# Optimization experiments

Measured on AMD Instinct MI355X. Metric: run time of the kernel, lower is better.

Reference implementation:

```python
import jax, jax.numpy as jnp
import numpy as np

N_DRUG, N_PROT = 20000, 8000
D_DRUG, D_PROT = 300, 1280
HIDDEN, OUT = 512, 5
N_EDGE, N_LBL = 500000, 200000


def setup_inputs() -> dict:
    key = jax.random.key(0)
    ks = jax.random.split(key, 12)
    inp = {
        "x_drug": jax.random.normal(ks[0], (N_DRUG, D_DRUG), dtype=jnp.float32),
        "x_prot": jax.random.normal(ks[1], (N_PROT, D_PROT), dtype=jnp.float32),
        "edge_src": jax.random.randint(ks[2], (N_EDGE,), 0, N_DRUG, dtype=jnp.int32),
        "edge_dst": jax.random.randint(ks[3], (N_EDGE,), 0, N_PROT, dtype=jnp.int32),
        "lbl_src": jax.random.randint(ks[4], (N_LBL,), 0, N_DRUG, dtype=jnp.int32),
        "lbl_dst": jax.random.randint(ks[5], (N_LBL,), 0, N_PROT, dtype=jnp.int32),
        # SAGEConv params: lin_l (on aggregated src msgs, with bias), lin_r (on dst, no bias)
        "W_l": jax.random.normal(ks[6], (HIDDEN, D_DRUG), dtype=jnp.float32) / np.sqrt(D_DRUG),
        "b_l": jnp.zeros((HIDDEN,), dtype=jnp.float32),
        "W_r": jax.random.normal(ks[7], (HIDDEN, D_PROT), dtype=jnp.float32) / np.sqrt(D_PROT),
        # final edge classifier Linear(D_DRUG + HIDDEN, OUT)
        "W_lin": jax.random.normal(ks[8], (OUT, D_DRUG + HIDDEN), dtype=jnp.float32) / np.sqrt(D_DRUG + HIDDEN),
        "b_lin": jnp.zeros((OUT,), dtype=jnp.float32),
    }
    return inp


def reference(x_drug, x_prot, edge_src, edge_dst, lbl_src, lbl_dst,
              W_l, b_l, W_r, W_lin, b_lin):
    # --- bipartite SAGEConv((drug, protein)) with default mean aggregation ---
    msg = x_drug[edge_src]                                   # [E, D_DRUG] gather
    agg = jax.ops.segment_sum(msg, edge_dst, num_segments=N_PROT)   # [N_PROT, D_DRUG]
    cnt = jax.ops.segment_sum(jnp.ones((edge_dst.shape[0],), jnp.float32),
                              edge_dst, num_segments=N_PROT)
    mean = agg / jnp.clip(cnt, 1.0, None)[:, None]           # mean over in-neighbors
    prot_emb_all = mean @ W_l.T + b_l + x_prot @ W_r.T       # [N_PROT, HIDDEN]

    # --- gather endpoints for labeled edges, concat, linear ---
    drug_emb = x_drug[lbl_src]                               # [L, D_DRUG]
    prot_emb = prot_emb_all[lbl_dst]                         # [L, HIDDEN]
    edge_emb = jnp.concatenate([drug_emb, prot_emb], axis=1) # [L, D_DRUG+HIDDEN]
    return edge_emb @ W_lin.T + b_lin                        # [L, OUT]
```

## Files before the change

kernel.cpp:

```cpp
#include <hip/hip_runtime.h>

#define N_DRUG 20000
#define N_PROT 8000
#define D_DRUG 300
#define D_PROT 1280
#define HIDDEN 512
#define OUT_D  5
#define N_EDGE 500000
#define N_LBL  200000
#define WLD    812
#define CAP    128
#define OVF_MAX 65536
#define CNT_STRIDE 32
#define SCAT_B 245

__global__ void k_fold_zero(const float* __restrict__ W_l, const float* __restrict__ W_r,
                            const float* __restrict__ W_lin, const float* __restrict__ b_l,
                            float* __restrict__ A, float* __restrict__ B, float* __restrict__ c,
                            float4* __restrict__ cntz, int* __restrict__ novf) {
    int b = blockIdx.x;
    if (b < 248) {
        int t  = b * 256 + threadIdx.x;
        int e  = t >> 3;
        int j  = t & 7;
        int h0 = j * 64;
        const int nA = OUT_D * D_DRUG;
        const int nB = OUT_D * D_PROT;
        float s = 0.f;
        if (e < nA) {
            int o = e / D_DRUG, k = e - o * D_DRUG;
            const float* wp = W_lin + o * WLD + D_DRUG + h0;
            const float* w  = W_l + (size_t)h0 * D_DRUG + k;
#pragma unroll 8
            for (int h = 0; h < 64; ++h) s += wp[h] * w[h * D_DRUG];
        } else if (e < nA + nB) {
            int u = e - nA;
            int o = u / D_PROT, k = u - o * D_PROT;
            const float* wp = W_lin + o * WLD + D_DRUG + h0;
            const float* w  = W_r + (size_t)h0 * D_PROT + k;
#pragma unroll 8
            for (int h = 0; h < 64; ++h) s += wp[h] * w[h * D_PROT];
        } else if (e < nA + nB + OUT_D) {
            int o = e - nA - nB;
            const float* wp = W_lin + o * WLD + D_DRUG + h0;
#pragma unroll 8
            for (int h = 0; h < 64; ++h) s += wp[h] * b_l[h0 + h];
        }
        s += __shfl_xor(s, 1, 64);
        s += __shfl_xor(s, 2, 64);
        s += __shfl_xor(s, 4, 64);
        if (j == 0) {
            if (e < nA)                     A[e] = s;
            else if (e < nA + nB)           B[e - nA] = s;
            else if (e < nA + nB + OUT_D)   c[e - nA - nB] = s;
        }
    } else {
        int idx = (b - 248) * 256 + threadIdx.x;
        cntz[idx] = make_float4(0.f, 0.f, 0.f, 0.f);
        if (idx == 0) *novf = 0;
    }
}

__global__ void k_scatter_dense(const float* __restrict__ x_drug, const float* __restrict__ x_prot,
                                const int* __restrict__ edge_src, const int* __restrict__ edge_dst,
                                const float* __restrict__ A, const float* __restrict__ B,
                                const float* __restrict__ c, const float* __restrict__ W_lin,
                                int* __restrict__ cnt, int* __restrict__ novf,
                                int* __restrict__ bucket, int* __restrict__ ovf,
                                float* __restrict__ P_A, float* __restrict__ drugO,
                                float* __restrict__ protO) {
    int b = blockIdx.x;
    if (b < SCAT_B) {
        int base = b * 2048 + threadIdx.x;
#pragma unroll
        for (int i = 0; i < 8; ++i) {
            int e = base + i * 256;
            if (e < N_EDGE) {
                int s = edge_src[e], d = edge_dst[e];
                int r = atomicAdd(&cnt[d * CNT_STRIDE], 1);
                if (r < CAP) {
                    bucket[d * CAP + r] = s;
                } else {
                    int o = atomicAdd(novf, 1);
                    if (o < OVF_MAX) { ovf[2 * o] = d; ovf[2 * o + 1] = s; }
                }
            }
        }
    } else if (b < SCAT_B + 1250) {
        int gid = (b - SCAT_B) * 256 + threadIdx.x;
        int row = gid >> 4;
        int sub = threadIdx.x & 15;
        const float4* xr = (const float4*)(x_drug + (size_t)row * D_DRUG);
        float acc[10];
#pragma unroll
        for (int i = 0; i < 10; ++i) acc[i] = 0.f;
        for (int k = sub; k < D_DRUG / 4; k += 16) {
            float4 x = xr[k];
#pragma unroll
            for (int o = 0; o < OUT_D; ++o) {
                float4 a = ((const float4*)(A + o * D_DRUG))[k];
                acc[o] += x.x * a.x + x.y * a.y + x.z * a.z + x.w * a.w;
                float4 w = ((const float4*)(W_lin + o * WLD))[k];
                acc[5 + o] += x.x * w.x + x.y * w.y + x.z * w.z + x.w * w.w;
            }
        }
#pragma unroll
        for (int i = 0; i < 10; ++i) {
            float v = acc[i];
            for (int m = 8; m; m >>= 1) v += __shfl_xor(v, m, 64);
            acc[i] = v;
        }
        if (sub < OUT_D) {
            P_A[row * OUT_D + sub]   = acc[sub];
            drugO[row * OUT_D + sub] = acc[5 + sub];
        }
    } else {
        int wave = ((b - SCAT_B - 1250) * 256 + threadIdx.x) >> 6;
        int lane = threadIdx.x & 63;
        const float4* xr = (const float4*)(x_prot + (size_t)wave * D_PROT);
        float acc[OUT_D] = {0.f, 0.f, 0.f, 0.f, 0.f};
        for (int k = lane; k < D_PROT / 4; k += 64) {
            float4 x = xr[k];
#pragma unroll
            for (int o = 0; o < OUT_D; ++o) {
                float4 bb = ((const float4*)(B + o * D_PROT))[k];
                acc[o] += x.x * bb.x + x.y * bb.y + x.z * bb.z + x.w * bb.w;
            }
        }
#pragma unroll
        for (int o = 0; o < OUT_D; ++o) {
            float v = acc[o];
            for (int off = 32; off; off >>= 1) v += __shfl_xor(v, off, 64);
            acc[o] = v;
        }
        if (lane < OUT_D) protO[wave * OUT_D + lane] = acc[lane] + c[lane];
    }
}

__global__ void k_gather(const int* __restrict__ cnt, const int* __restrict__ novf,
                         const int* __restrict__ bucket, const int* __restrict__ ovf,
                         const float* __restrict__ P_A, float* __restrict__ protO) {
    int wave = (blockIdx.x * blockDim.x + threadIdx.x) >> 6;
    int lane = threadIdx.x & 63;
    if (wave >= N_PROT) return;
    int deg = cnt[wave * CNT_STRIDE];
    int m = deg < CAP ? deg : CAP;
    float acc[OUT_D] = {0.f, 0.f, 0.f, 0.f, 0.f};
    const int* br = &bucket[wave * CAP];
    for (int j = lane; j < m; j += 64) {
        const float* p = &P_A[br[j] * OUT_D];
#pragma unroll
        for (int o = 0; o < OUT_D; ++o) acc[o] += p[o];
    }
    if (deg > CAP) {
        int nv = *novf; if (nv > OVF_MAX) nv = OVF_MAX;
        for (int j = lane; j < nv; j += 64) {
            if (ovf[2 * j] == wave) {
                const float* p = &P_A[ovf[2 * j + 1] * OUT_D];
#pragma unroll
                for (int o = 0; o < OUT_D; ++o) acc[o] += p[o];
            }
        }
    }
#pragma unroll
    for (int o = 0; o < OUT_D; ++o) {
        float v = acc[o];
        for (int off = 32; off; off >>= 1) v += __shfl_xor(v, off, 64);
        acc[o] = v;
    }
    if (lane < OUT_D)
        protO[wave * OUT_D + lane] += acc[lane] / fmaxf((float)deg, 1.f);
}

__global__ void k_final(const int* __restrict__ lbl_src, const int* __restrict__ lbl_dst,
                        const float* __restrict__ drugO, const float* __restrict__ protO,
                        const float* __restrict__ b_lin, float* __restrict__ out) {
    int l = blockIdx.x * blockDim.x + threadIdx.x;
    if (l >= N_LBL) return;
    int s = lbl_src[l], d = lbl_dst[l];
    const float* dr = &drugO[s * OUT_D];
    const float* pr = &protO[d * OUT_D];
    float* op = &out[(size_t)l * OUT_D];
    op[0] = dr[0] + pr[0] + b_lin[0];
    op[1] = dr[1] + pr[1] + b_lin[1];
    op[2] = dr[2] + pr[2] + b_lin[2];
    op[3] = dr[3] + pr[3] + b_lin[3];
    op[4] = dr[4] + pr[4] + b_lin[4];
}

extern "C" void kernel_launch(void* const* d_in, const int* in_sizes, int n_in,
                              void* d_out, int out_size, void* d_ws, size_t ws_size,
                              hipStream_t stream) {
    const float* x_drug   = (const float*)d_in[0];
    const float* x_prot   = (const float*)d_in[1];
    const int*   edge_src = (const int*)d_in[2];
    const int*   edge_dst = (const int*)d_in[3];
    const int*   lbl_src  = (const int*)d_in[4];
    const int*   lbl_dst  = (const int*)d_in[5];
    const float* W_l      = (const float*)d_in[6];
    const float* b_l      = (const float*)d_in[7];
    const float* W_r      = (const float*)d_in[8];
    const float* W_lin    = (const float*)d_in[9];
    const float* b_lin    = (const float*)d_in[10];
    float* out = (float*)d_out;

    char* ws = (char*)d_ws;
    int*   cnt    = (int*)  (ws + 0);
    int*   novf   = (int*)  (ws + 1048576);
    float* A      = (float*)(ws + 1048592);
    float* B      = (float*)(ws + 1054592);
    float* c      = (float*)(ws + 1080192);
    float* P_A    = (float*)(ws + 1080320);
    float* drugO  = (float*)(ws + 1480320);
    float* protO  = (float*)(ws + 1880320);
    int*   bucket = (int*)  (ws + 2040320);
    int*   ovf    = (int*)  (ws + 6136320);

    k_fold_zero<<<504, 256, 0, stream>>>(W_l, W_r, W_lin, b_l, A, B, c,
                                         (float4*)cnt, novf);
    k_scatter_dense<<<3495, 256, 0, stream>>>(x_drug, x_prot, edge_src, edge_dst,
                                              A, B, c, W_lin, cnt, novf, bucket, ovf,
                                              P_A, drugO, protO);
    k_gather<<<2000, 256, 0, stream>>>(cnt, novf, bucket, ovf, P_A, protO);
    k_final<<<(N_LBL + 255) / 256, 256, 0, stream>>>(lbl_src, lbl_dst, drugO, protO, b_lin, out);
}
```

Measured before the change: 164.5 us.

## Replace bucket scatter+gather with direct float atomic aggregation of projected messages

Instead of bucketing edge source indices per protein and gathering them in a separate kernel, each edge now atomically adds the drug's 5-wide projected vector plus a count into a small per-protein accumulator. The mean division moves into the final kernel, and the drug projection is split into its own kernel so P_A is ready before the scatter. This removes the gather kernel, the bucket and overflow buffers, and the overflow scan. The cost is six float atomics per edge and a dependency that serialises the drug projection ahead of the scatter, and float atomic ordering makes the summation order nondeterministic.

```diff
diff --git a/kernel.cpp b/kernel.cpp
--- a/kernel.cpp
+++ b/kernel.cpp
@@ -9,15 +9,14 @@
 #define N_EDGE 500000
 #define N_LBL  200000
 #define WLD    812
-#define CAP    128
-#define OVF_MAX 65536
-#define CNT_STRIDE 32
+#define AGG_S  8
+#define PA_S   8
 #define SCAT_B 245
 
 __global__ void k_fold_zero(const float* __restrict__ W_l, const float* __restrict__ W_r,
                             const float* __restrict__ W_lin, const float* __restrict__ b_l,
                             float* __restrict__ A, float* __restrict__ B, float* __restrict__ c,
-                            float4* __restrict__ cntz, int* __restrict__ novf) {
+                            float4* __restrict__ aggz) {
     int b = blockIdx.x;
     if (b < 248) {
         int t  = b * 256 + threadIdx.x;
@@ -56,19 +55,50 @@
         }
     } else {
         int idx = (b - 248) * 256 + threadIdx.x;
-        cntz[idx] = make_float4(0.f, 0.f, 0.f, 0.f);
-        if (idx == 0) *novf = 0;
+        if (idx < (N_PROT * AGG_S) / 4)
+            aggz[idx] = make_float4(0.f, 0.f, 0.f, 0.f);
     }
 }
 
-__global__ void k_scatter_dense(const float* __restrict__ x_drug, const float* __restrict__ x_prot,
-                                const int* __restrict__ edge_src, const int* __restrict__ edge_dst,
-                                const float* __restrict__ A, const float* __restrict__ B,
-                                const float* __restrict__ c, const float* __restrict__ W_lin,
-                                int* __restrict__ cnt, int* __restrict__ novf,
-                                int* __restrict__ bucket, int* __restrict__ ovf,
-                                float* __restrict__ P_A, float* __restrict__ drugO,
-                                float* __restrict__ protO) {
+__global__ void k_drug(const float* __restrict__ x_drug, const float* __restrict__ A,
+                       const float* __restrict__ W_lin, const float* __restrict__ b_lin,
+                       float* __restrict__ P_A, float* __restrict__ drugO) {
+    int gid = blockIdx.x * 256 + threadIdx.x;
+    int row = gid >> 4;
+    int sub = threadIdx.x & 15;
+    const float4* xr = (const float4*)(x_drug + (size_t)row * D_DRUG);
+    float acc[10];
+#pragma unroll
+    for (int i = 0; i < 10; ++i) acc[i] = 0.f;
+    for (int k = sub; k < D_DRUG / 4; k += 16) {
+        float4 x = xr[k];
+#pragma unroll
+        for (int o = 0; o < OUT_D; ++o) {
+            float4 a = ((const float4*)(A + o * D_DRUG))[k];
+            acc[o] += x.x * a.x + x.y * a.y + x.z * a.z + x.w * a.w;
+            float4 w = ((const float4*)(W_lin + o * WLD))[k];
+            acc[5 + o] += x.x * w.x + x.y * w.y + x.z * w.z + x.w * w.w;
+        }
+    }
+#pragma unroll
+    for (int i = 0; i < 10; ++i) {
+        float v = acc[i];
+        for (int m = 8; m; m >>= 1) v += __shfl_xor(v, m, 64);
+        acc[i] = v;
+    }
+    if (sub < OUT_D) {
+        P_A[(size_t)row * PA_S + sub]    = acc[sub];
+        drugO[(size_t)row * OUT_D + sub] = acc[5 + sub] + b_lin[sub];
+    } else if (sub < PA_S) {
+        P_A[(size_t)row * PA_S + sub] = 0.f;
+    }
+}
+
+__global__ void k_scatter_prot(const float* __restrict__ x_prot,
+                               const int* __restrict__ edge_src, const int* __restrict__ edge_dst,
+                               const float* __restrict__ B, const float* __restrict__ c,
+                               const float* __restrict__ P_A, float* __restrict__ agg,
+                               float* __restrict__ protO) {
     int b = blockIdx.x;
     if (b < SCAT_B) {
         int base = b * 2048 + threadIdx.x;
@@ -77,45 +107,20 @@
             int e = base + i * 256;
             if (e < N_EDGE) {
                 int s = edge_src[e], d = edge_dst[e];
-                int r = atomicAdd(&cnt[d * CNT_STRIDE], 1);
-                if (r < CAP) {
-                    bucket[d * CAP + r] = s;
-                } else {
-                    int o = atomicAdd(novf, 1);
-                    if (o < OVF_MAX) { ovf[2 * o] = d; ovf[2 * o + 1] = s; }
-                }
+                const float* p = P_A + (size_t)s * PA_S;
+                float4 p4 = *(const float4*)p;
+                float  p5 = p[4];
+                float* ag = agg + (size_t)d * AGG_S;
+                unsafeAtomicAdd(&ag[0], p4.x);
+                unsafeAtomicAdd(&ag[1], p4.y);
+                unsafeAtomicAdd(&ag[2], p4.z);
+                unsafeAtomicAdd(&ag[3], p4.w);
+                unsafeAtomicAdd(&ag[4], p5);
+                unsafeAtomicAdd(&ag[5], 1.0f);
             }
         }
-    } else if (b < SCAT_B + 1250) {
-        int gid = (b - SCAT_B) * 256 + threadIdx.x;
-        int row = gid >> 4;
-        int sub = threadIdx.x & 15;
-        const float4* xr = (const float4*)(x_drug + (size_t)row * D_DRUG);
-        float acc[10];
-#pragma unroll
-        for (int i = 0; i < 10; ++i) acc[i] = 0.f;
-        for (int k = sub; k < D_DRUG / 4; k += 16) {
-            float4 x = xr[k];
-#pragma unroll
-            for (int o = 0; o < OUT_D; ++o) {
-                float4 a = ((const float4*)(A + o * D_DRUG))[k];
-                acc[o] += x.x * a.x + x.y * a.y + x.z * a.z + x.w * a.w;
-                float4 w = ((const float4*)(W_lin + o * WLD))[k];
-                acc[5 + o] += x.x * w.x + x.y * w.y + x.z * w.z + x.w * w.w;
-            }
-        }
-#pragma unroll
-        for (int i = 0; i < 10; ++i) {
-            float v = acc[i];
-            for (int m = 8; m; m >>= 1) v += __shfl_xor(v, m, 64);
-            acc[i] = v;
-        }
-        if (sub < OUT_D) {
-            P_A[row * OUT_D + sub]   = acc[sub];
-            drugO[row * OUT_D + sub] = acc[5 + sub];
-        }
     } else {
-        int wave = ((b - SCAT_B - 1250) * 256 + threadIdx.x) >> 6;
+        int wave = ((b - SCAT_B) * 256 + threadIdx.x) >> 6;
         int lane = threadIdx.x & 63;
         const float4* xr = (const float4*)(x_prot + (size_t)wave * D_PROT);
         float acc[OUT_D] = {0.f, 0.f, 0.f, 0.f, 0.f};
@@ -133,59 +138,28 @@
             for (int off = 32; off; off >>= 1) v += __shfl_xor(v, off, 64);
             acc[o] = v;
         }
-        if (lane < OUT_D) protO[wave * OUT_D + lane] = acc[lane] + c[lane];
+        if (lane < OUT_D) protO[(size_t)wave * OUT_D + lane] = acc[lane] + c[lane];
     }
-}
-
-__global__ void k_gather(const int* __restrict__ cnt, const int* __restrict__ novf,
-                         const int* __restrict__ bucket, const int* __restrict__ ovf,
-                         const float* __restrict__ P_A, float* __restrict__ protO) {
-    int wave = (blockIdx.x * blockDim.x + threadIdx.x) >> 6;
-    int lane = threadIdx.x & 63;
-    if (wave >= N_PROT) return;
-    int deg = cnt[wave * CNT_STRIDE];
-    int m = deg < CAP ? deg : CAP;
-    float acc[OUT_D] = {0.f, 0.f, 0.f, 0.f, 0.f};
-    const int* br = &bucket[wave * CAP];
-    for (int j = lane; j < m; j += 64) {
-        const float* p = &P_A[br[j] * OUT_D];
-#pragma unroll
-        for (int o = 0; o < OUT_D; ++o) acc[o] += p[o];
-    }
-    if (deg > CAP) {
-        int nv = *novf; if (nv > OVF_MAX) nv = OVF_MAX;
-        for (int j = lane; j < nv; j += 64) {
-            if (ovf[2 * j] == wave) {
-                const float* p = &P_A[ovf[2 * j + 1] * OUT_D];
-#pragma unroll
-                for (int o = 0; o < OUT_D; ++o) acc[o] += p[o];
-            }
-        }
-    }
-#pragma unroll
-    for (int o = 0; o < OUT_D; ++o) {
-        float v = acc[o];
-        for (int off = 32; off; off >>= 1) v += __shfl_xor(v, off, 64);
-        acc[o] = v;
-    }
-    if (lane < OUT_D)
-        protO[wave * OUT_D + lane] += acc[lane] / fmaxf((float)deg, 1.f);
 }
 
 __global__ void k_final(const int* __restrict__ lbl_src, const int* __restrict__ lbl_dst,
                         const float* __restrict__ drugO, const float* __restrict__ protO,
-                        const float* __restrict__ b_lin, float* __restrict__ out) {
+                        const float* __restrict__ agg, float* __restrict__ out) {
     int l = blockIdx.x * blockDim.x + threadIdx.x;
     if (l >= N_LBL) return;
     int s = lbl_src[l], d = lbl_dst[l];
-    const float* dr = &drugO[s * OUT_D];
-    const float* pr = &protO[d * OUT_D];
+    const float* dr = &drugO[(size_t)s * OUT_D];
+    const float* pr = &protO[(size_t)d * OUT_D];
+    const float* ag = &agg[(size_t)d * AGG_S];
+    float4 a4 = *(const float4*)ag;
+    float  a5 = ag[4];
+    float  inv = 1.0f / fmaxf(ag[5], 1.0f);
     float* op = &out[(size_t)l * OUT_D];
-    op[0] = dr[0] + pr[0] + b_lin[0];
-    op[1] = dr[1] + pr[1] + b_lin[1];
-    op[2] = dr[2] + pr[2] + b_lin[2];
-    op[3] = dr[3] + pr[3] + b_lin[3];
-    op[4] = dr[4] + pr[4] + b_lin[4];
+    op[0] = dr[0] + pr[0] + a4.x * inv;
+    op[1] = dr[1] + pr[1] + a4.y * inv;
+    op[2] = dr[2] + pr[2] + a4.z * inv;
+    op[3] = dr[3] + pr[3] + a4.w * inv;
+    op[4] = dr[4] + pr[4] + a5 * inv;
 }
 
 extern "C" void kernel_launch(void* const* d_in, const int* in_sizes, int n_in,
@@ -205,22 +179,17 @@
     float* out = (float*)d_out;
 
     char* ws = (char*)d_ws;
-    int*   cnt    = (int*)  (ws + 0);
-    int*   novf   = (int*)  (ws + 1048576);
-    float* A      = (float*)(ws + 1048592);
-    float* B      = (float*)(ws + 1054592);
-    float* c      = (float*)(ws + 1080192);
-    float* P_A    = (float*)(ws + 1080320);
-    float* drugO  = (float*)(ws + 1480320);
-    float* protO  = (float*)(ws + 1880320);
-    int*   bucket = (int*)  (ws + 2040320);
-    int*   ovf    = (int*)  (ws + 6136320);
+    float* agg    = (float*)(ws + 0);
+    float* A      = (float*)(ws + 256000);
+    float* B      = (float*)(ws + 262000);
+    float* c      = (float*)(ws + 287600);
+    float* P_A    = (float*)(ws + 287632);
+    float* drugO  = (float*)(ws + 927632);
+    float* protO  = (float*)(ws + 1327632);
 
-    k_fold_zero<<<504, 256, 0, stream>>>(W_l, W_r, W_lin, b_l, A, B, c,
-                                         (float4*)cnt, novf);
-    k_scatter_dense<<<3495, 256, 0, stream>>>(x_drug, x_prot, edge_src, edge_dst,
-                                              A, B, c, W_lin, cnt, novf, bucket, ovf,
-                                              P_A, drugO, protO);
-    k_gather<<<2000, 256, 0, stream>>>(cnt, novf, bucket, ovf, P_A, protO);
-    k_final<<<(N_LBL + 255) / 256, 256, 0, stream>>>(lbl_src, lbl_dst, drugO, protO, b_lin, out);
+    k_fold_zero<<<311, 256, 0, stream>>>(W_l, W_r, W_lin, b_l, A, B, c, (float4*)agg);
+    k_drug<<<1250, 256, 0, stream>>>(x_drug, A, W_lin, b_lin, P_A, drugO);
+    k_scatter_prot<<<SCAT_B + 2000, 256, 0, stream>>>(x_prot, edge_src, edge_dst,
+                                                      B, c, P_A, agg, protO);
+    k_final<<<(N_LBL + 255) / 256, 256, 0, stream>>>(lbl_src, lbl_dst, drugO, protO, agg, out);
 }
```

Result: slower. 290.7 us (+76.7%).
